# Kernel optimization log

Hardware: AMD Instinct MI355X
Metric: run time of the kernel (lower is better)

## Reference

```python
import jax, jax.numpy as jnp
import numpy as np

N_QUBITS = 8
DIM = 2 ** N_QUBITS  # 256 state-vector dim
EMBED = 512
FFN = 2048
B, S = 4, 8192


def setup_inputs() -> dict:
    key = jax.random.key(0)
    k_x, k_w1, k_b1, k_w2, k_b2 = jax.random.split(key, 5)
    # Random-layer unitary: QR of a complex Gaussian matrix (Haar-like).
    rng = np.random.default_rng(0)
    A = rng.standard_normal((DIM, DIM)) + 1j * rng.standard_normal((DIM, DIM))
    Q, _ = np.linalg.qr(A)
    U_re = jnp.asarray(Q.real, dtype=jnp.float32)
    U_im = jnp.asarray(Q.imag, dtype=jnp.float32)
    x = jax.random.normal(k_x, (B, S, EMBED), dtype=jnp.float32)
    # torch nn.Linear params: y = x @ W.T + b
    W1 = jax.random.normal(k_w1, (FFN, N_QUBITS), dtype=jnp.float32) / np.sqrt(N_QUBITS)
    b1 = jax.random.normal(k_b1, (FFN,), dtype=jnp.float32) * 0.01
    W2 = jax.random.normal(k_w2, (EMBED, FFN), dtype=jnp.float32) / np.sqrt(FFN)
    b2 = jax.random.normal(k_b2, (EMBED,), dtype=jnp.float32) * 0.01
    return {"x": x, "U_re": U_re, "U_im": U_im, "W1": W1, "b1": b1, "W2": W2, "b2": b2}


def _pauliz_expectations(U_re, U_im, n_qubits):
    # Device starts in |0...0>, so post-layer state is column 0 of U.
    psi_re = U_re[:, 0]
    psi_im = U_im[:, 0]
    probs = psi_re * psi_re + psi_im * psi_im            # [2^n]
    p = probs.reshape((2,) * n_qubits)                   # wire i -> axis i
    zs = []
    for i in range(n_qubits):
        pm = jnp.moveaxis(p, i, 0).reshape(2, -1).sum(axis=-1)
        zs.append(pm[0] - pm[1])                         # <Z_i> = P(0) - P(1)
    return jnp.stack(zs)                                 # [n_qubits]


def reference(x, U_re, U_im, W1, b1, W2, b2):
    b, s, _ = x.shape
    n_qubits = W1.shape[1]
    z = _pauliz_expectations(U_re, U_im, n_qubits)       # identical for every token
    feat = jnp.broadcast_to(z, (b, s, n_qubits))         # [B, S, n_qubits]
    # dropout is identity at inference
    h = jax.nn.relu(jnp.einsum('bsq,fq->bsf', feat, W1) + b1)
    out = jnp.einsum('bsf,ef->bse', h, W2) + b2          # [B, S, embed]
    return out
```

## Files before the change

kernel.cpp:

```cpp
#include <hip/hip_runtime.h>

#define DIM   256
#define NQ    8
#define EMBED 512
#define FFN   2048
#define ROWS  (4 * 8192)
#define OUT_ELEMS (ROWS * EMBED)
#define OUT_VEC4  (EMBED / 4)
#define OUT_TOTAL4 (OUT_ELEMS / 4)

__global__ void k_compute_h(const float* __restrict__ U_re,
                            const float* __restrict__ U_im,
                            const float* __restrict__ W1,
                            const float* __restrict__ b1,
                            float* __restrict__ h) {
    __shared__ float probs[DIM];
    __shared__ float z[NQ];
    int t = threadIdx.x;

    float re = U_re[t * DIM];
    float im = U_im[t * DIM];
    probs[t] = re * re + im * im;
    __syncthreads();

    if (t < NQ) {
        float s = 0.f;
        int shift = NQ - 1 - t;
        for (int k = 0; k < DIM; ++k) {
            float p = probs[k];
            s += ((k >> shift) & 1) ? -p : p;
        }
        z[t] = s;
    }
    __syncthreads();

    float zr[NQ];
#pragma unroll
    for (int q = 0; q < NQ; ++q) zr[q] = z[q];

#pragma unroll
    for (int r = 0; r < FFN / 256; ++r) {
        int f = r * 256 + t;
        const float4* w = (const float4*)(W1 + f * NQ);
        float4 w0 = w[0], w1 = w[1];
        float acc = b1[f];
        acc += zr[0] * w0.x + zr[1] * w0.y + zr[2] * w0.z + zr[3] * w0.w;
        acc += zr[4] * w1.x + zr[5] * w1.y + zr[6] * w1.z + zr[7] * w1.w;
        h[f] = fmaxf(acc, 0.f);
    }
}

__global__ void k_compute_out(const float* __restrict__ W2,
                              const float* __restrict__ b2,
                              const float* __restrict__ h,
                              float* __restrict__ ov) {
    int e = blockIdx.x;
    int t = threadIdx.x;
    const float4* row = (const float4*)(W2 + (size_t)e * FFN);
    const float4* h4  = (const float4*)h;

    float4 a0 = row[t],       hb0 = h4[t];
    float4 a1 = row[256 + t], hb1 = h4[256 + t];
    float p = a0.x * hb0.x + a0.y * hb0.y + a0.z * hb0.z + a0.w * hb0.w
            + a1.x * hb1.x + a1.y * hb1.y + a1.z * hb1.z + a1.w * hb1.w;

#pragma unroll
    for (int off = 32; off > 0; off >>= 1)
        p += __shfl_down(p, off, 64);

    __shared__ float wsum[4];
    if ((t & 63) == 0) wsum[t >> 6] = p;
    __syncthreads();
    if (t == 0)
        ov[e] = wsum[0] + wsum[1] + wsum[2] + wsum[3] + b2[e];
}

__global__ void k_broadcast(const float* __restrict__ ov,
                            float* __restrict__ out) {
    const float4* ov4 = (const float4*)ov;
    float4* out4 = (float4*)out;
    int idx = blockIdx.x * blockDim.x + threadIdx.x;
    int stride = gridDim.x * blockDim.x;
    float4 v = ov4[idx & (OUT_VEC4 - 1)];
    for (; idx < OUT_TOTAL4; idx += stride)
        out4[idx] = v;
}

extern "C" void kernel_launch(void* const* d_in, const int* in_sizes, int n_in,
                              void* d_out, int out_size, void* d_ws, size_t ws_size,
                              hipStream_t stream) {
    const float* U_re = (const float*)d_in[1];
    const float* U_im = (const float*)d_in[2];
    const float* W1   = (const float*)d_in[3];
    const float* b1   = (const float*)d_in[4];
    const float* W2   = (const float*)d_in[5];
    const float* b2   = (const float*)d_in[6];
    float* out = (float*)d_out;

    float* h  = (float*)d_ws;
    float* ov = h + FFN;

    k_compute_h  <<<1,     256, 0, stream>>>(U_re, U_im, W1, b1, h);
    k_compute_out<<<EMBED, 256, 0, stream>>>(W2, b2, h, ov);
    k_broadcast  <<<2048,  256, 0, stream>>>(ov, out);
}
```

Before: 126.7 us.

## Fuse h computation into per-output kernel and parallelize Pauli-Z reduction

Merges the single-block h kernel into the W2 GEMV kernel, so every one of the 512 blocks redundantly recomputes the Pauli-Z expectations and the 2048-wide hidden vector in shared memory. This drops one kernel launch and the serial 8-thread loop in favour of a shuffle-based reduction. The broadcast grid is also doubled. The cost is redundant reads of U and W1 in every block, which mostly hit cache.

```diff
diff --git a/kernel.cpp b/kernel.cpp
--- a/kernel.cpp
+++ b/kernel.cpp
@@ -9,35 +9,45 @@
 #define OUT_VEC4  (EMBED / 4)
 #define OUT_TOTAL4 (OUT_ELEMS / 4)
 
-__global__ void k_compute_h(const float* __restrict__ U_re,
-                            const float* __restrict__ U_im,
-                            const float* __restrict__ W1,
-                            const float* __restrict__ b1,
-                            float* __restrict__ h) {
-    __shared__ float probs[DIM];
-    __shared__ float z[NQ];
+__global__ void k_ov(const float* __restrict__ U_re,
+                     const float* __restrict__ U_im,
+                     const float* __restrict__ W1,
+                     const float* __restrict__ b1,
+                     const float* __restrict__ W2,
+                     const float* __restrict__ b2,
+                     float* __restrict__ ov) {
     int t = threadIdx.x;
+    int e = blockIdx.x;
 
     float re = U_re[t * DIM];
     float im = U_im[t * DIM];
-    probs[t] = re * re + im * im;
+    float p  = re * re + im * im;
+
+    float zp[NQ];
+#pragma unroll
+    for (int q = 0; q < NQ; ++q)
+        zp[q] = ((t >> (NQ - 1 - q)) & 1) ? -p : p;
+#pragma unroll
+    for (int off = 32; off > 0; off >>= 1) {
+#pragma unroll
+        for (int q = 0; q < NQ; ++q)
+            zp[q] += __shfl_down(zp[q], off, 64);
+    }
+    __shared__ float zw[4][NQ];
+    if ((t & 63) == 0) {
+#pragma unroll
+        for (int q = 0; q < NQ; ++q) zw[t >> 6][q] = zp[q];
+    }
     __syncthreads();
-
-    if (t < NQ) {
-        float s = 0.f;
-        int shift = NQ - 1 - t;
-        for (int k = 0; k < DIM; ++k) {
-            float p = probs[k];
-            s += ((k >> shift) & 1) ? -p : p;
-        }
-        z[t] = s;
-    }
+    __shared__ float zs[NQ];
+    if (t < NQ) zs[t] = zw[0][t] + zw[1][t] + zw[2][t] + zw[3][t];
     __syncthreads();
 
     float zr[NQ];
 #pragma unroll
-    for (int q = 0; q < NQ; ++q) zr[q] = z[q];
+    for (int q = 0; q < NQ; ++q) zr[q] = zs[q];
 
+    __shared__ float h[FFN];
 #pragma unroll
     for (int r = 0; r < FFN / 256; ++r) {
         int f = r * 256 + t;
@@ -48,28 +58,19 @@
         acc += zr[4] * w1.x + zr[5] * w1.y + zr[6] * w1.z + zr[7] * w1.w;
         h[f] = fmaxf(acc, 0.f);
     }
-}
+    __syncthreads();
 
-__global__ void k_compute_out(const float* __restrict__ W2,
-                              const float* __restrict__ b2,
-                              const float* __restrict__ h,
-                              float* __restrict__ ov) {
-    int e = blockIdx.x;
-    int t = threadIdx.x;
     const float4* row = (const float4*)(W2 + (size_t)e * FFN);
     const float4* h4  = (const float4*)h;
-
     float4 a0 = row[t],       hb0 = h4[t];
     float4 a1 = row[256 + t], hb1 = h4[256 + t];
-    float p = a0.x * hb0.x + a0.y * hb0.y + a0.z * hb0.z + a0.w * hb0.w
-            + a1.x * hb1.x + a1.y * hb1.y + a1.z * hb1.z + a1.w * hb1.w;
-
+    float acc = a0.x * hb0.x + a0.y * hb0.y + a0.z * hb0.z + a0.w * hb0.w
+              + a1.x * hb1.x + a1.y * hb1.y + a1.z * hb1.z + a1.w * hb1.w;
 #pragma unroll
     for (int off = 32; off > 0; off >>= 1)
-        p += __shfl_down(p, off, 64);
-
+        acc += __shfl_down(acc, off, 64);
     __shared__ float wsum[4];
-    if ((t & 63) == 0) wsum[t >> 6] = p;
+    if ((t & 63) == 0) wsum[t >> 6] = acc;
     __syncthreads();
     if (t == 0)
         ov[e] = wsum[0] + wsum[1] + wsum[2] + wsum[3] + b2[e];
@@ -97,10 +98,8 @@
     const float* b2   = (const float*)d_in[6];
     float* out = (float*)d_out;
 
-    float* h  = (float*)d_ws;
-    float* ov = h + FFN;
+    float* ov = (float*)d_ws;
 
-    k_compute_h  <<<1,     256, 0, stream>>>(U_re, U_im, W1, b1, h);
-    k_compute_out<<<EMBED, 256, 0, stream>>>(W2, b2, h, ov);
-    k_broadcast  <<<2048,  256, 0, stream>>>(ov, out);
+    k_ov       <<<EMBED, 256, 0, stream>>>(U_re, U_im, W1, b1, W2, b2, ov);
+    k_broadcast<<<4096,  256, 0, stream>>>(ov, out);
 }
```

Result: faster. 120.8 us (-4.7%).
